# Performance work log

Measured on AMD Instinct MI355X. Metric: run time of the kernel, lower is better.

## Reference

```python
import jax, jax.numpy as jnp
import numpy as np

B, S, D = 2, 2048, 1024
H = 16
HD = D // H  # head_dim = 64
NEG = -1e30  # finite stand-in for -inf; masked entries are zeroed after softmax so math matches


def setup_inputs() -> dict:
    key = jax.random.key(0)
    ks = jax.random.split(key, 10)
    q = jax.random.normal(ks[0], (B, S, D), dtype=jnp.float32)
    k = jax.random.normal(ks[1], (B, S, D), dtype=jnp.float32)
    v = jax.random.normal(ks[2], (B, S, D), dtype=jnp.float32)
    mask = jax.random.randint(ks[3], (B, S), 0, 2).astype(bool)
    s = 1.0 / np.sqrt(D)
    Wq = jax.random.uniform(ks[4], (D, D), jnp.float32, -s, s)
    bq = jax.random.uniform(ks[5], (D,), jnp.float32, -s, s)
    Wk = jax.random.uniform(ks[6], (D, D), jnp.float32, -s, s)
    bk = jax.random.uniform(ks[7], (D,), jnp.float32, -s, s)
    Wv = jax.random.uniform(ks[8], (D, D), jnp.float32, -s, s)
    bv = jax.random.uniform(ks[9], (D,), jnp.float32, -s, s)
    return {"q": q, "k": k, "v": v, "mask": mask,
            "Wq": Wq, "bq": bq, "Wk": Wk, "bk": bk, "Wv": Wv, "bv": bv}


def _split_heads(x):
    # [B,S,D] -> [H,B,S,HD]  (matches permute(2,0,1,3) in torch)
    return x.reshape(B, S, H, HD).transpose(2, 0, 1, 3)


def reference(q, k, v, mask, Wq, bq, Wk, bk, Wv, bv):
    mq = _split_heads(q @ Wq.T + bq)
    mk = _split_heads(k @ Wk.T + bk)
    mv = _split_heads(v @ Wv.T + bv)
    # scores: [H,B,Sq,Sk]
    scores = jnp.einsum('hbqd,hbkd->hbqk', mq, mk) / jnp.sqrt(jnp.float32(HD))
    pair_mask = (mask[:, :, None] & mask[:, None, :])[None]  # [1,B,S,S]
    scores = jnp.where(pair_mask, scores, NEG)
    attn = jax.nn.softmax(scores, axis=-1)
    attn = jnp.where(pair_mask, attn, 0.0)
    out = jnp.einsum('hbqk,hbkd->hbqd', attn, mv)
    # [H,B,S,HD] -> [B,S,D]
    return out.transpose(1, 2, 0, 3).reshape(B, S, H * HD)
```

## Files before the change

### kernel.cpp

```cpp
#include <hip/hip_runtime.h>
#include <math.h>

#define B_ 2
#define S_ 2048
#define D_ 1024
#define H_ 16
#define HD_ 64

typedef __bf16 bf16_t;
typedef bf16_t bf16x8 __attribute__((ext_vector_type(8)));
typedef bf16_t bf16x4v __attribute__((ext_vector_type(4)));
typedef float f32x4 __attribute__((ext_vector_type(4)));

#define GLOBAL_LOAD_LDS16(gp, lp)                                              \
    __builtin_amdgcn_global_load_lds(                                          \
        (const __attribute__((address_space(1))) void*)(gp),                   \
        (__attribute__((address_space(3))) void*)(lp), 16, 0, 0)

__global__ __launch_bounds__(256) void cvt_kernel(
    const float* __restrict__ q, const float* __restrict__ k,
    const float* __restrict__ v, const float* __restrict__ wq,
    const float* __restrict__ wk, const float* __restrict__ wv,
    const int* __restrict__ msk,
    bf16_t* __restrict__ qb, bf16_t* __restrict__ kb, bf16_t* __restrict__ vb,
    bf16_t* __restrict__ wqb, bf16_t* __restrict__ wkb, bf16_t* __restrict__ wvb,
    float* __restrict__ kbias)
{
    const int y = blockIdx.y;
    size_t idx = ((size_t)blockIdx.x * 256 + threadIdx.x) * 4;

    if (y == 6) {
        if (idx >= (size_t)B_ * S_) return;
        int4 mi = *(const int4*)(msk + idx);
        float4 o4;
        o4.x = mi.x ? -8.0f : -1e30f;
        o4.y = mi.y ? -8.0f : -1e30f;
        o4.z = mi.z ? -8.0f : -1e30f;
        o4.w = mi.w ? -8.0f : -1e30f;
        *(float4*)(kbias + idx) = o4;
        return;
    }

    const float* src;
    bf16_t* dst;
    size_t n;
    switch (y) {
        case 0: src = q;  dst = qb;  n = (size_t)B_ * S_ * D_; break;
        case 1: src = k;  dst = kb;  n = (size_t)B_ * S_ * D_; break;
        case 2: src = v;  dst = vb;  n = (size_t)B_ * S_ * D_; break;
        case 3: src = wq; dst = wqb; n = (size_t)D_ * D_;      break;
        case 4: src = wk; dst = wkb; n = (size_t)D_ * D_;      break;
        default: src = wv; dst = wvb; n = (size_t)D_ * D_;     break;
    }
    if (idx >= n) return;
    float4 f = *(const float4*)(src + idx);
    bf16x4v o;
    o[0] = (bf16_t)f.x; o[1] = (bf16_t)f.y;
    o[2] = (bf16_t)f.z; o[3] = (bf16_t)f.w;
    *(bf16x4v*)(dst + idx) = o;
}

__global__ __launch_bounds__(256) void proj_mfma(
    const bf16_t* __restrict__ X0, const bf16_t* __restrict__ X1,
    const bf16_t* __restrict__ X2, const bf16_t* __restrict__ W0,
    const bf16_t* __restrict__ W1, const bf16_t* __restrict__ W2,
    const float* __restrict__ b0, const float* __restrict__ b1,
    const float* __restrict__ b2, bf16_t* __restrict__ o0,
    bf16_t* __restrict__ o1, bf16_t* __restrict__ o2)
{
    __shared__ __align__(16) bf16_t As[128 * 32];
    __shared__ __align__(16) bf16_t Bs[128 * 32];

    const int z = blockIdx.z;
    const bf16_t* X = (z == 0) ? X0 : (z == 1) ? X1 : X2;
    const bf16_t* W = (z == 0) ? W0 : (z == 1) ? W1 : W2;
    const float* bias = (z == 0) ? b0 : (z == 1) ? b1 : b2;
    bf16_t* out = (z == 0) ? o0 : (z == 1) ? o1 : o2;
    const float oscale = (z == 0) ? 0.125f : 1.0f;

    const int tid  = threadIdx.x;
    const int w    = tid >> 6;
    const int lane = tid & 63;
    const int L    = lane & 15;
    const int quad = lane >> 4;
    const int wr   = (w >> 1) * 64;
    const int wc   = (w & 1) * 64;
    const int row0 = blockIdx.x * 128;
    const int col0 = blockIdx.y * 128;

    const int lr = lane >> 2;
    const int lc = (lane & 3) * 8;

    f32x4 acc[4][4];
    #pragma unroll
    for (int i = 0; i < 4; ++i)
        #pragma unroll
        for (int j = 0; j < 4; ++j) {
            acc[i][j][0] = 0.f; acc[i][j][1] = 0.f;
            acc[i][j][2] = 0.f; acc[i][j][3] = 0.f;
        }

    for (int k0 = 0; k0 < D_; k0 += 32) {
        __syncthreads();
        #pragma unroll
        for (int i = 0; i < 2; ++i) {
            const int rA = i * 64 + w * 16;
            GLOBAL_LOAD_LDS16(X + (size_t)(row0 + rA + lr) * D_ + k0 + lc,
                              &As[rA * 32]);
            GLOBAL_LOAD_LDS16(W + (size_t)(col0 + rA + lr) * D_ + k0 + lc,
                              &Bs[rA * 32]);
        }
        __syncthreads();

        bf16x8 aF[4], bF[4];
        #pragma unroll
        for (int t = 0; t < 4; ++t) {
            aF[t] = *(const bf16x8*)&As[(wr + t * 16 + L) * 32 + quad * 8];
            bF[t] = *(const bf16x8*)&Bs[(wc + t * 16 + L) * 32 + quad * 8];
        }
        #pragma unroll
        for (int mt = 0; mt < 4; ++mt)
            #pragma unroll
            for (int nt = 0; nt < 4; ++nt)
                acc[mt][nt] = __builtin_amdgcn_mfma_f32_16x16x32_bf16(
                    aF[mt], bF[nt], acc[mt][nt], 0, 0, 0);
    }

    #pragma unroll
    for (int nt = 0; nt < 4; ++nt) {
        const int j  = col0 + wc + nt * 16 + L;
        const float bval = bias[j];
        const int h  = j >> 6;
        const int hd = j & 63;
        #pragma unroll
        for (int mt = 0; mt < 4; ++mt)
            #pragma unroll
            for (int r = 0; r < 4; ++r) {
                const int n = row0 + wr + mt * 16 + quad * 4 + r;
                const int b = n >> 11;
                const int s = n & (S_ - 1);
                out[((((size_t)b * H_ + h) * S_ + s) * HD_) + hd] =
                    (bf16_t)((acc[mt][nt][r] + bval) * oscale);
            }
    }
}

__global__ __launch_bounds__(256) void transpose_v(
    const bf16_t* __restrict__ mv, bf16_t* __restrict__ vt)
{
    __shared__ bf16_t tile[64][72];
    const int s0 = blockIdx.x * 64;
    const int bh = blockIdx.y;
    const int t  = threadIdx.x;

    const bf16_t* src = mv + ((size_t)bh * S_ + s0) * HD_;
    {
        int srow = t >> 2, c16 = (t & 3) * 16;
        bf16x8 a = *(const bf16x8*)(src + srow * HD_ + c16);
        bf16x8 b = *(const bf16x8*)(src + srow * HD_ + c16 + 8);
        *(bf16x8*)&tile[srow][c16]     = a;
        *(bf16x8*)&tile[srow][c16 + 8] = b;
    }
    __syncthreads();

    const int d  = t & 63;
    const int sc = (t >> 6) * 16;
    unsigned int w[8];
    #pragma unroll
    for (int j = 0; j < 8; ++j) {
        unsigned short lo = *(const unsigned short*)&tile[sc + 2*j][d];
        unsigned short hi = *(const unsigned short*)&tile[sc + 2*j + 1][d];
        w[j] = (unsigned int)lo | ((unsigned int)hi << 16);
    }
    bf16_t* dst = vt + ((size_t)bh * HD_ + d) * S_ + s0 + sc;
    uint4 u0; u0.x = w[0]; u0.y = w[1]; u0.z = w[2]; u0.w = w[3];
    uint4 u1; u1.x = w[4]; u1.y = w[5]; u1.z = w[6]; u1.w = w[7];
    ((uint4*)dst)[0] = u0;
    ((uint4*)dst)[1] = u1;
}

__global__ __launch_bounds__(256) void attn_kernel(
    const bf16_t* __restrict__ Q, const bf16_t* __restrict__ K,
    const bf16_t* __restrict__ Vt, const float* __restrict__ kbias,
    const int* __restrict__ mask, float* __restrict__ out)
{
    constexpr int LD = 72;
    __shared__ bf16_t Ks[64 * LD];
    __shared__ bf16_t Vs[64 * LD];
    __shared__ bf16_t Pt[4][32 * LD];

    const int tid  = threadIdx.x;
    const int w    = tid >> 6;
    const int lane = tid & 63;
    const int L    = lane & 15;
    const int quad = lane >> 4;
    const int h    = blockIdx.y;
    const int b    = blockIdx.z;
    const int bh   = b * H_ + h;
    const int q0   = blockIdx.x * 128;

    const bf16_t* kbase = K  + (size_t)bh * S_ * HD_;
    const bf16_t* vbase = Vt + (size_t)bh * HD_ * S_;
    const float*  bbase = kbias + b * S_;
    const int*    mrow  = mask + b * S_;

    const int sr = tid >> 3;
    const int sc2 = (tid & 7) * 8;

    bf16x8 aQ[2][2];
    #pragma unroll
    for (int qb = 0; qb < 2; ++qb) {
        const bf16_t* qp = Q + ((size_t)bh * S_ + q0 + w * 32 + qb * 16 + L) * HD_;
        aQ[qb][0] = *(const bf16x8*)(qp + quad * 8);
        aQ[qb][1] = *(const bf16x8*)(qp + 32 + quad * 8);
    }

    f32x4 o[2][4];
    #pragma unroll
    for (int qb = 0; qb < 2; ++qb)
        #pragma unroll
        for (int f = 0; f < 4; ++f) {
            o[qb][f][0]=0.f; o[qb][f][1]=0.f; o[qb][f][2]=0.f; o[qb][f][3]=0.f;
        }
    float l_[2] = {0.f, 0.f};

    bf16x8 kr0, kr1, vr0, vr1;
    f32x4  bias_n[4];
    {
        kr0 = *(const bf16x8*)(kbase + (size_t)sr * HD_ + sc2);
        kr1 = *(const bf16x8*)(kbase + (size_t)(sr + 32) * HD_ + sc2);
        vr0 = *(const bf16x8*)(vbase + (size_t)sr * S_ + sc2);
        vr1 = *(const bf16x8*)(vbase + (size_t)(sr + 32) * S_ + sc2);
        #pragma unroll
        for (int f = 0; f < 4; ++f)
            bias_n[f] = *(const f32x4*)(bbase + f * 16 + quad * 4);
    }

    for (int kt = 0; kt < S_; kt += 64) {
        __syncthreads();
        *(bf16x8*)&Ks[sr * LD + sc2]        = kr0;
        *(bf16x8*)&Ks[(sr + 32) * LD + sc2] = kr1;
        *(bf16x8*)&Vs[sr * LD + sc2]        = vr0;
        *(bf16x8*)&Vs[(sr + 32) * LD + sc2] = vr1;
        f32x4 bias_c[4];
        #pragma unroll
        for (int f = 0; f < 4; ++f) bias_c[f] = bias_n[f];
        __syncthreads();

        if (kt + 64 < S_) {
            const int kn = kt + 64;
            kr0 = *(const bf16x8*)(kbase + (size_t)(kn + sr) * HD_ + sc2);
            kr1 = *(const bf16x8*)(kbase + (size_t)(kn + sr + 32) * HD_ + sc2);
            vr0 = *(const bf16x8*)(vbase + (size_t)sr * S_ + kn + sc2);
            vr1 = *(const bf16x8*)(vbase + (size_t)(sr + 32) * S_ + kn + sc2);
            #pragma unroll
            for (int f = 0; f < 4; ++f)
                bias_n[f] = *(const f32x4*)(bbase + kn + f * 16 + quad * 4);
        }

        bf16x8 aK[4][2];
        #pragma unroll
        for (int f = 0; f < 4; ++f) {
            aK[f][0] = *(const bf16x8*)&Ks[(f * 16 + L) * LD + quad * 8];
            aK[f][1] = *(const bf16x8*)&Ks[(f * 16 + L) * LD + 32 + quad * 8];
        }

        bf16_t* pw = &Pt[w][0];
        #pragma unroll
        for (int qb = 0; qb < 2; ++qb) {
            #pragma unroll
            for (int f = 0; f < 4; ++f) {
                f32x4 z = bias_c[f];
                z = __builtin_amdgcn_mfma_f32_16x16x32_bf16(aK[f][0], aQ[qb][0], z, 0, 0, 0);
                z = __builtin_amdgcn_mfma_f32_16x16x32_bf16(aK[f][1], aQ[qb][1], z, 0, 0, 0);
                float e0 = __expf(z[0]);
                float e1 = __expf(z[1]);
                float e2 = __expf(z[2]);
                float e3 = __expf(z[3]);
                l_[qb] += (e0 + e1) + (e2 + e3);
                bf16x4v p4;
                p4[0] = (bf16_t)e0; p4[1] = (bf16_t)e1;
                p4[2] = (bf16_t)e2; p4[3] = (bf16_t)e3;
                *(bf16x4v*)&pw[(qb * 16 + L) * LD + f * 16 + quad * 4] = p4;
            }
        }

        bf16x8 aP[2][2];
        #pragma unroll
        for (int qb = 0; qb < 2; ++qb) {
            aP[qb][0] = *(const bf16x8*)&pw[(qb * 16 + L) * LD + quad * 8];
            aP[qb][1] = *(const bf16x8*)&pw[(qb * 16 + L) * LD + 32 + quad * 8];
        }

        #pragma unroll
        for (int f = 0; f < 4; ++f) {
            bf16x8 bV0 = *(const bf16x8*)&Vs[(f * 16 + L) * LD + quad * 8];
            bf16x8 bV1 = *(const bf16x8*)&Vs[(f * 16 + L) * LD + 32 + quad * 8];
            #pragma unroll
            for (int qb = 0; qb < 2; ++qb) {
                o[qb][f] = __builtin_amdgcn_mfma_f32_16x16x32_bf16(aP[qb][0], bV0, o[qb][f], 0, 0, 0);
                o[qb][f] = __builtin_amdgcn_mfma_f32_16x16x32_bf16(aP[qb][1], bV1, o[qb][f], 0, 0, 0);
            }
        }
    }

    #pragma unroll
    for (int qb = 0; qb < 2; ++qb) {
        float t = l_[qb];
        t += __shfl_xor(t, 16);
        t += __shfl_xor(t, 32);
        int qv = mrow[q0 + w * 32 + qb * 16 + L];
        l_[qb] = (qv && t > 0.f) ? (1.0f / t) : 0.0f;
    }

    #pragma unroll
    for (int qb = 0; qb < 2; ++qb) {
        float inv[4];
        #pragma unroll
        for (int r = 0; r < 4; ++r)
            inv[r] = __shfl(l_[qb], quad * 4 + r);
        float* obase = out + ((size_t)b * S_ + q0 + w * 32 + qb * 16 + quad * 4) * D_ + h * HD_;
        #pragma unroll
        for (int f = 0; f < 4; ++f)
            #pragma unroll
            for (int r = 0; r < 4; ++r)
                obase[r * D_ + f * 16 + L] = o[qb][f][r] * inv[r];
    }
}

extern "C" void kernel_launch(void* const* d_in, const int* in_sizes, int n_in,
                              void* d_out, int out_size, void* d_ws, size_t ws_size,
                              hipStream_t stream)
{
    const float* q    = (const float*)d_in[0];
    const float* k    = (const float*)d_in[1];
    const float* v    = (const float*)d_in[2];
    const int*   mask = (const int*)d_in[3];
    const float* Wq   = (const float*)d_in[4];
    const float* bq   = (const float*)d_in[5];
    const float* Wk   = (const float*)d_in[6];
    const float* bk   = (const float*)d_in[7];
    const float* Wv   = (const float*)d_in[8];
    const float* bv   = (const float*)d_in[9];
    float* out = (float*)d_out;

    const size_t PE = (size_t)B_ * S_ * D_;
    const size_t WE = (size_t)D_ * D_;

    bf16_t* qb    = (bf16_t*)d_ws;
    bf16_t* kb    = qb + PE;
    bf16_t* vb    = kb + PE;
    bf16_t* wqb   = vb + PE;
    bf16_t* wkb   = wqb + WE;
    bf16_t* wvb   = wkb + WE;
    bf16_t* mq    = wvb + WE;
    bf16_t* mk    = mq + PE;
    bf16_t* mv    = mk + PE;
    bf16_t* vt    = mv + PE;
    float*  kbias = (float*)(vt + PE);

    dim3 cgrid(PE / (256 * 4), 7);
    cvt_kernel<<<cgrid, 256, 0, stream>>>(q, k, v, Wq, Wk, Wv, mask,
                                          qb, kb, vb, wqb, wkb, wvb, kbias);

    dim3 pgrid(4096 / 128, 1024 / 128, 3);
    proj_mfma<<<pgrid, 256, 0, stream>>>(qb, kb, vb, wqb, wkb, wvb,
                                         bq, bk, bv, mq, mk, mv);

    dim3 tgrid(S_ / 64, B_ * H_);
    transpose_v<<<tgrid, 256, 0, stream>>>(mv, vt);

    dim3 agrid(S_ / 128, H_, B_);
    attn_kernel<<<agrid, 256, 0, stream>>>(mq, mk, vt, kbias, mask, out);
}
```

Baseline: 211.6 us.

## Fuse V transpose into projection epilogue and switch softmax to exp2

```diff
diff --git a/kernel.cpp b/kernel.cpp
--- a/kernel.cpp
+++ b/kernel.cpp
@@ -6,6 +6,8 @@
 #define D_ 1024
 #define H_ 16
 #define HD_ 64
+
+#define LOG2E 1.44269504088896f
 
 typedef __bf16 bf16_t;
 typedef bf16_t bf16x8 __attribute__((ext_vector_type(8)));
@@ -32,11 +34,12 @@
     if (y == 6) {
         if (idx >= (size_t)B_ * S_) return;
         int4 mi = *(const int4*)(msk + idx);
+        const float vb_ = -8.0f * LOG2E;
         float4 o4;
-        o4.x = mi.x ? -8.0f : -1e30f;
-        o4.y = mi.y ? -8.0f : -1e30f;
-        o4.z = mi.z ? -8.0f : -1e30f;
-        o4.w = mi.w ? -8.0f : -1e30f;
+        o4.x = mi.x ? vb_ : -1e30f;
+        o4.y = mi.y ? vb_ : -1e30f;
+        o4.z = mi.z ? vb_ : -1e30f;
+        o4.w = mi.w ? vb_ : -1e30f;
         *(float4*)(kbias + idx) = o4;
         return;
     }
@@ -76,7 +79,7 @@
     const bf16_t* W = (z == 0) ? W0 : (z == 1) ? W1 : W2;
     const float* bias = (z == 0) ? b0 : (z == 1) ? b1 : b2;
     bf16_t* out = (z == 0) ? o0 : (z == 1) ? o1 : o2;
-    const float oscale = (z == 0) ? 0.125f : 1.0f;
+    const float oscale = (z == 0) ? 0.125f * LOG2E : 1.0f;
 
     const int tid  = threadIdx.x;
     const int w    = tid >> 6;
@@ -126,57 +129,44 @@
                     aF[mt], bF[nt], acc[mt][nt], 0, 0, 0);
     }
 
-    #pragma unroll
-    for (int nt = 0; nt < 4; ++nt) {
-        const int j  = col0 + wc + nt * 16 + L;
-        const float bval = bias[j];
-        const int h  = j >> 6;
-        const int hd = j & 63;
-        #pragma unroll
-        for (int mt = 0; mt < 4; ++mt)
-            #pragma unroll
-            for (int r = 0; r < 4; ++r) {
-                const int n = row0 + wr + mt * 16 + quad * 4 + r;
+    if (z == 2) {
+        #pragma unroll
+        for (int nt = 0; nt < 4; ++nt) {
+            const int j  = col0 + wc + nt * 16 + L;
+            const float bval = bias[j];
+            const int h  = j >> 6;
+            const int hd = j & 63;
+            #pragma unroll
+            for (int mt = 0; mt < 4; ++mt) {
+                const int n = row0 + wr + mt * 16 + quad * 4;
                 const int b = n >> 11;
                 const int s = n & (S_ - 1);
-                out[((((size_t)b * H_ + h) * S_ + s) * HD_) + hd] =
-                    (bf16_t)((acc[mt][nt][r] + bval) * oscale);
+                bf16x4v r4;
+                #pragma unroll
+                for (int r = 0; r < 4; ++r)
+                    r4[r] = (bf16_t)(acc[mt][nt][r] + bval);
+                *(bf16x4v*)(out + (((size_t)b * H_ + h) * HD_ + hd) * S_ + s) = r4;
             }
-    }
-}
-
-__global__ __launch_bounds__(256) void transpose_v(
-    const bf16_t* __restrict__ mv, bf16_t* __restrict__ vt)
-{
-    __shared__ bf16_t tile[64][72];
-    const int s0 = blockIdx.x * 64;
-    const int bh = blockIdx.y;
-    const int t  = threadIdx.x;
-
-    const bf16_t* src = mv + ((size_t)bh * S_ + s0) * HD_;
-    {
-        int srow = t >> 2, c16 = (t & 3) * 16;
-        bf16x8 a = *(const bf16x8*)(src + srow * HD_ + c16);
-        bf16x8 b = *(const bf16x8*)(src + srow * HD_ + c16 + 8);
-        *(bf16x8*)&tile[srow][c16]     = a;
-        *(bf16x8*)&tile[srow][c16 + 8] = b;
-    }
-    __syncthreads();
-
-    const int d  = t & 63;
-    const int sc = (t >> 6) * 16;
-    unsigned int w[8];
-    #pragma unroll
-    for (int j = 0; j < 8; ++j) {
-        unsigned short lo = *(const unsigned short*)&tile[sc + 2*j][d];
-        unsigned short hi = *(const unsigned short*)&tile[sc + 2*j + 1][d];
-        w[j] = (unsigned int)lo | ((unsigned int)hi << 16);
-    }
-    bf16_t* dst = vt + ((size_t)bh * HD_ + d) * S_ + s0 + sc;
-    uint4 u0; u0.x = w[0]; u0.y = w[1]; u0.z = w[2]; u0.w = w[3];
-    uint4 u1; u1.x = w[4]; u1.y = w[5]; u1.z = w[6]; u1.w = w[7];
-    ((uint4*)dst)[0] = u0;
-    ((uint4*)dst)[1] = u1;
+        }
+    } else {
+        #pragma unroll
+        for (int nt = 0; nt < 4; ++nt) {
+            const int j  = col0 + wc + nt * 16 + L;
+            const float bval = bias[j];
+            const int h  = j >> 6;
+            const int hd = j & 63;
+            #pragma unroll
+            for (int mt = 0; mt < 4; ++mt)
+                #pragma unroll
+                for (int r = 0; r < 4; ++r) {
+                    const int n = row0 + wr + mt * 16 + quad * 4 + r;
+                    const int b = n >> 11;
+                    const int s = n & (S_ - 1);
+                    out[((((size_t)b * H_ + h) * S_ + s) * HD_) + hd] =
+                        (bf16_t)((acc[mt][nt][r] + bval) * oscale);
+                }
+        }
+    }
 }
 
 __global__ __launch_bounds__(256) void attn_kernel(
@@ -204,7 +194,7 @@
     const float*  bbase = kbias + b * S_;
     const int*    mrow  = mask + b * S_;
 
-    const int sr = tid >> 3;
+    const int sr  = tid >> 3;
     const int sc2 = (tid & 7) * 8;
 
     bf16x8 aQ[2][2];
@@ -273,10 +263,10 @@
                 f32x4 z = bias_c[f];
                 z = __builtin_amdgcn_mfma_f32_16x16x32_bf16(aK[f][0], aQ[qb][0], z, 0, 0, 0);
                 z = __builtin_amdgcn_mfma_f32_16x16x32_bf16(aK[f][1], aQ[qb][1], z, 0, 0, 0);
-                float e0 = __expf(z[0]);
-                float e1 = __expf(z[1]);
-                float e2 = __expf(z[2]);
-                float e3 = __expf(z[3]);
+                float e0 = exp2f(z[0]);
+                float e1 = exp2f(z[1]);
+                float e2 = exp2f(z[2]);
+                float e3 = exp2f(z[3]);
                 l_[qb] += (e0 + e1) + (e2 + e3);
                 bf16x4v p4;
                 p4[0] = (bf16_t)e0; p4[1] = (bf16_t)e1;
@@ -355,8 +345,7 @@
     bf16_t* wvb   = wkb + WE;
     bf16_t* mq    = wvb + WE;
     bf16_t* mk    = mq + PE;
-    bf16_t* mv    = mk + PE;
-    bf16_t* vt    = mv + PE;
+    bf16_t* vt    = mk + PE;
     float*  kbias = (float*)(vt + PE);
 
     dim3 cgrid(PE / (256 * 4), 7);
@@ -365,10 +354,7 @@
 
     dim3 pgrid(4096 / 128, 1024 / 128, 3);
     proj_mfma<<<pgrid, 256, 0, stream>>>(qb, kb, vb, wqb, wkb, wvb,
-                                         bq, bk, bv, mq, mk, mv);
-
-    dim3 tgrid(S_ / 64, B_ * H_);
-    transpose_v<<<tgrid, 256, 0, stream>>>(mv, vt);
+                                         bq, bk, bv, mq, mk, vt);
 
     dim3 agrid(S_ / 128, H_, B_);
     attn_kernel<<<agrid, 256, 0, stream>>>(mq, mk, vt, kbias, mask, out);
```

New measurement: 227.7 us. +7.6%, slower.
